# Kernel optimization log

Measured on AMD Instinct MI355X. Metric: run time of the kernel, lower is better.

## Reference

```python
import jax, jax.numpy as jnp
import numpy as np
from jax import lax

N_CLS = 3
ALPHA = 2
NMS = True


def _make_level(key, B, A, D, H, W, P, counts):
    k1, k2, k3, k4, k5 = jax.random.split(key, 5)
    C = N_CLS * A
    logit = jax.random.normal(k1, (B, C, D, H, W), dtype=jnp.float32)
    # valid positive coords use d,h,w >= 1 so padded writes to (0,0,0,0) never collide
    a = jax.random.randint(k2, (B, P), 0, A)
    d = jax.random.randint(k3, (B, P), 1, D)
    h = jax.random.randint(k4, (B, P), 1, H)
    w = jax.random.randint(k5, (B, P), 1, W)
    labels = jax.random.randint(jax.random.fold_in(key, 7), (B, P), 0, N_CLS)
    valid = jnp.arange(P)[None, :] < jnp.asarray(counts)[:, None]  # [B,P]
    coord = jnp.stack([a, d, h, w], axis=-1)
    coord = jnp.where(valid[..., None], coord, -1).astype(jnp.int32)
    # ground-truth prob map: -1 = negative, class id (float) at positive voxels
    prob_gt = -jnp.ones((B, A, D, H, W), dtype=jnp.float32)
    cs = jnp.where(valid[..., None], coord, 0)
    b_idx = jnp.arange(B)[:, None]
    vals = jnp.where(valid, labels.astype(jnp.float32), -1.0)
    prob_gt = prob_gt.at[b_idx, cs[..., 0], cs[..., 1], cs[..., 2], cs[..., 3]].set(vals)
    return logit, prob_gt, coord


def setup_inputs() -> dict:
    key = jax.random.key(0)
    kA, kB = jax.random.split(key)
    logit0, prob_gt0, coord0 = _make_level(kA, 4, 3, 64, 64, 64, 128, [128, 64, 32, 0])
    logit1, prob_gt1, coord1 = _make_level(kB, 4, 3, 32, 32, 32, 128, [64, 16, 8, 128])
    weight_cls = jnp.array([1.0, 1.5, 2.0], dtype=jnp.float32)
    return {
        "logit0": logit0, "logit1": logit1,
        "prob_gt0": prob_gt0, "prob_gt1": prob_gt1,
        "coord0": coord0, "coord1": coord1,
        "weight_cls": weight_cls,
    }


def _level_loss(logit, prob_gt, coord_gt, weight_cls):
    B, C, D, H, W = logit.shape
    A = C // N_CLS
    logit = logit.reshape(B, N_CLS, A, D, H, W)
    logp = jax.nn.log_softmax(logit, axis=1)
    nll = -logp                      # [B,N_cls,A,D,H,W]
    prob = jnp.exp(logp)
    nll_neg = nll[:, 0]              # [B,A,D,H,W]
    prob_neg = prob[:, 0]
    negmask = (prob_gt == -1).astype(logit.dtype)
    if NMS:
        mp = lax.reduce_window(nll_neg, -jnp.inf, lax.max,
                               (1, 1, 3, 3, 3), (1, 1, 1, 1, 1),
                               [(0, 0), (0, 0), (1, 1), (1, 1), (1, 1)])
        negmask = negmask * lax.stop_gradient((mp == nll_neg).astype(logit.dtype))
    w_neg = (1.0 - lax.stop_gradient(prob_neg)) ** ALPHA * negmask
    loss_neg = jnp.sum(nll_neg * w_neg)
    count_neg = jnp.sum(w_neg)
    # positives: ragged coord gather, masked instead of per-sample python loop
    valid = coord_gt[:, :, 0] > -1                       # [B,P]
    c = jnp.where(valid[..., None], coord_gt, 0)         # safe coords
    a, d, h, w = c[..., 0], c[..., 1], c[..., 2], c[..., 3]
    b_idx = jnp.arange(B)[:, None]
    cls = prob_gt[b_idx, a, d, h, w].astype(jnp.int32)   # class id at positives
    cls = jnp.where(valid, cls, 0)
    p_t = prob[b_idx, cls, a, d, h, w]
    nll_t = nll[b_idx, cls, a, d, h, w]
    w_pos = ((1.0 - lax.stop_gradient(p_t)) ** ALPHA
             * weight_cls[cls] * valid.astype(logit.dtype))
    loss_pos = jnp.sum(nll_t * w_pos)
    count_pos = jnp.sum(w_pos)
    return loss_pos, loss_neg, count_pos, count_neg


def reference(logit0, logit1, prob_gt0, prob_gt1, coord0, coord1, weight_cls):
    lp0, ln0, cp0, cn0 = _level_loss(logit0, prob_gt0, coord0, weight_cls)
    lp1, ln1, cp1, cn1 = _level_loss(logit1, prob_gt1, coord1, weight_cls)
    return jnp.stack([lp0 + lp1, ln0 + ln1, cp0 + cp1, cn0 + cn1])
```

## Files before the change

### kernel.cpp

```cpp
#include <hip/hip_runtime.h>
#include <math.h>

#define NEG_INF (-INFINITY)

__device__ __forceinline__ float nll3(float l0, float l1, float l2) {
    float m = fmaxf(l0, fmaxf(l1, l2));
    float e0 = __expf(l0 - m);
    float e1 = __expf(l1 - m);
    float e2 = __expf(l2 - m);
    return __logf(e0 + e1 + e2) - (l0 - m);
}

template<int W, int NR, int TD, int D, int H>
__device__ void neg_strip_p2(int uid, int lane,
                             const float* __restrict__ logit,
                             const float* __restrict__ pg,
                             float2* __restrict__ slot) {
    constexpr int LR = W / 4;
    constexpr int NI = NR + 2;
    constexpr int HG = H / NR;
    constexpr int DT = D / TD;
    const int q = lane % LR;
    const int g = lane / LR;

    int t = uid;
    const int hg = t % HG; t /= HG;
    const int dt = t % DT; t /= DT;
    const int ba = t;
    const int a = ba % 3, b = ba / 3;
    const int h0 = hg * NR, d0 = dt * TD;
    const int HW = H * W;

    const long S = (long)D * HW;
    const float* lb  = logit + ((long)b * 9 + a) * S;
    const long  cs   = 3 * S;
    const float* pgb = pg + (long)ba * S;

    const int jrow = h0 - 1 + g;
    const bool hv = (jrow >= 0) && (jrow < H) && (g < NI);
    const int hcl = min(max(jrow, 0), H - 1);
    const int rowoff = hcl * W + 4 * q;
    const int prowoff = (h0 + min(g, NR - 1)) * W + 4 * q;

    float4 A0, A1, A2, B0, B1, B2, C0, C1, C2;
    float4 GA, GB, GC;
    bool vA, vB, vC;

    {
        const float* p = lb + (long)max(d0 - 1, 0) * HW + rowoff;
        A0 = *(const float4*)p;
        A1 = *(const float4*)(p + cs);
        A2 = *(const float4*)(p + 2 * cs);
        vA = (d0 - 1 >= 0);
        const float* p2 = lb + (long)d0 * HW + rowoff;
        B0 = *(const float4*)p2;
        B1 = *(const float4*)(p2 + cs);
        B2 = *(const float4*)(p2 + 2 * cs);
        vB = true;
        GA = make_float4(0.f, 0.f, 0.f, 0.f);
        GB = make_float4(0.f, 0.f, 0.f, 0.f);
    }

    float vm0[4], vm1[4], cc1[4];
#pragma unroll
    for (int i = 0; i < 4; ++i) { vm0[i] = NEG_INF; vm1[i] = NEG_INF; cc1[i] = 0.f; }

    float loss = 0.f, cnt = 0.f;

#pragma unroll
    for (int s = 0; s <= TD + 1; ++s) {
        if (s <= TD - 1) {
            const int pd = d0 + 1 + s;
            const float* p = lb + (long)min(pd, D - 1) * HW + rowoff;
            C0 = *(const float4*)p;
            C1 = *(const float4*)(p + cs);
            C2 = *(const float4*)(p + 2 * cs);
            vC = (pd < D);
            GC = *(const float4*)(pgb + (long)(d0 + s) * HW + prowoff);
        } else {
            vC = false;
            C0 = C1 = C2 = make_float4(0.f, 0.f, 0.f, 0.f);
            GC = make_float4(0.f, 0.f, 0.f, 0.f);
        }

        float nvv[4];
        {
            const bool vv = vA && hv;
            nvv[0] = vv ? nll3(A0.x, A1.x, A2.x) : NEG_INF;
            nvv[1] = vv ? nll3(A0.y, A1.y, A2.y) : NEG_INF;
            nvv[2] = vv ? nll3(A0.z, A1.z, A2.z) : NEG_INF;
            nvv[3] = vv ? nll3(A0.w, A1.w, A2.w) : NEG_INF;
        }

        float le = __shfl(nvv[3], lane - 1);
        float re = __shfl(nvv[0], lane + 1);
        le = (q == 0)      ? NEG_INF : le;
        re = (q == LR - 1) ? NEG_INF : re;
        float rm[4];
        rm[0] = fmaxf(le,     fmaxf(nvv[0], nvv[1]));
        rm[1] = fmaxf(nvv[0], fmaxf(nvv[1], nvv[2]));
        rm[2] = fmaxf(nvv[1], fmaxf(nvv[2], nvv[3]));
        rm[3] = fmaxf(nvv[2], fmaxf(nvv[3], re));

        float rmA[4], rmB[4], ctr[4];
#pragma unroll
        for (int i = 0; i < 4; ++i) {
            rmA[i] = __shfl(rm[i],  lane + LR);
            rmB[i] = __shfl(rm[i],  lane + 2 * LR);
            ctr[i] = __shfl(nvv[i], lane + LR);
        }

        const float pgv[4] = {GA.x, GA.y, GA.z, GA.w};
#pragma unroll
        for (int i = 0; i < 4; ++i) {
            float hw2 = fmaxf(rm[i], fmaxf(rmA[i], rmB[i]));
            if (s >= 2 && g < NR && pgv[i] == -1.0f) {
                float mp = fmaxf(vm0[i], fmaxf(vm1[i], hw2));
                if (mp == cc1[i]) {
                    float pn = __expf(-cc1[i]);
                    float wn = (1.f - pn) * (1.f - pn);
                    loss += cc1[i] * wn;
                    cnt  += wn;
                }
            }
            vm0[i] = vm1[i]; vm1[i] = hw2; cc1[i] = ctr[i];
        }

        GA = GB; GB = GC;
        A0 = B0; A1 = B1; A2 = B2; vA = vB;
        B0 = C0; B1 = C1; B2 = C2; vB = vC;
    }

#pragma unroll
    for (int off = 32; off > 0; off >>= 1) {
        loss += __shfl_down(loss, off);
        cnt  += __shfl_down(cnt, off);
    }
    if (lane == 0) slot[uid] = make_float2(loss, cnt);
}

__device__ void pos_wave8(int sub, int lane,
                          const float* __restrict__ logit,
                          const float* __restrict__ prob_gt,
                          const int* __restrict__ coord,
                          const float* __restrict__ wcls,
                          float2* __restrict__ slot,
                          int D, int H, int W) {
    const int A = 3, P = 128;
    const long S = (long)D * H * W;
    const int i = sub * 64 + lane;
    const int b = i / P;
    const int* c = coord + (long)i * 4;
    const int a = c[0];
    float loss = 0.f, cnt = 0.f;
    if (a > -1) {
        const int d = c[1], h = c[2], w = c[3];
        const long s = ((long)d * H + h) * W + w;
        const int cls = (int)prob_gt[((long)b * A + a) * S + s];
        const float* lp = logit + ((long)b * 3 * A + a) * S + s;
        float l0 = lp[0];
        float l1 = lp[(long)A * S];
        float l2 = lp[2L * A * S];
        float m = fmaxf(l0, fmaxf(l1, l2));
        float e0 = __expf(l0 - m);
        float e1 = __expf(l1 - m);
        float e2 = __expf(l2 - m);
        float lsum = __logf(e0 + e1 + e2);
        float lc = (cls == 0) ? l0 : ((cls == 1) ? l1 : l2);
        float lpc = (lc - m) - lsum;
        float pt = __expf(lpc);
        float wp = (1.f - pt) * (1.f - pt) * wcls[cls];
        loss = (-lpc) * wp;
        cnt = wp;
    }
#pragma unroll
    for (int off = 32; off > 0; off >>= 1) {
        loss += __shfl_down(loss, off);
        cnt  += __shfl_down(cnt, off);
    }
    if (lane == 0) *slot = make_float2(loss, cnt);
}

#define NW0 3072
#define NW1 384
#define NWP 16
#define NUNEG (NW0 + NW1)
#define TOTAL_WAVES (NW0 + NW1 + NWP)

__global__ __launch_bounds__(256)
void mega_kernel(const float* __restrict__ logit0,
                 const float* __restrict__ logit1,
                 const float* __restrict__ pg0,
                 const float* __restrict__ pg1,
                 const int* __restrict__ coord0,
                 const int* __restrict__ coord1,
                 const float* __restrict__ wcls,
                 float2* __restrict__ ws) {
    const int gw = blockIdx.x * 4 + (threadIdx.x >> 6);
    const int lane = threadIdx.x & 63;
    float2* wsneg = ws;
    float2* wspos = ws + NUNEG;
    if (gw < NW0) {
        neg_strip_p2<64, 2, 8, 64, 64>(gw, lane, logit0, pg0, wsneg);
    } else if (gw < NW0 + NW1) {
        neg_strip_p2<32, 4, 8, 32, 32>(gw - NW0, lane, logit1, pg1, wsneg + NW0);
    } else if (gw < NW0 + NW1 + 8) {
        const int sub = gw - NW0 - NW1;
        pos_wave8(sub, lane, logit0, pg0, coord0, wcls, wspos + sub, 64, 64, 64);
    } else {
        const int sub = gw - NW0 - NW1 - 8;
        pos_wave8(sub, lane, logit1, pg1, coord1, wcls, wspos + 8 + sub, 32, 32, 32);
    }
}

__global__ __launch_bounds__(1024)
void final_reduce(const float2* __restrict__ ws, float* __restrict__ out) {
    const float2* wsneg = ws;
    const float2* wspos = ws + NUNEG;
    float ln = 0.f, cn = 0.f, lp = 0.f, cp = 0.f;
    for (int i = threadIdx.x; i < NUNEG; i += 1024) {
        float2 v = wsneg[i]; ln += v.x; cn += v.y;
    }
    if (threadIdx.x < NWP) {
        float2 v = wspos[threadIdx.x]; lp = v.x; cp = v.y;
    }
#pragma unroll
    for (int off = 32; off > 0; off >>= 1) {
        ln += __shfl_down(ln, off); cn += __shfl_down(cn, off);
        lp += __shfl_down(lp, off); cp += __shfl_down(cp, off);
    }
    __shared__ float s[16][4];
    const int wv = threadIdx.x >> 6;
    if ((threadIdx.x & 63) == 0) {
        s[wv][0] = ln; s[wv][1] = cn; s[wv][2] = lp; s[wv][3] = cp;
    }
    __syncthreads();
    if (threadIdx.x == 0) {
        float a = 0.f, b = 0.f, c = 0.f, d = 0.f;
#pragma unroll
        for (int i = 0; i < 16; ++i) {
            a += s[i][0]; b += s[i][1]; c += s[i][2]; d += s[i][3];
        }
        out[0] = c;
        out[1] = a;
        out[2] = d;
        out[3] = b;
    }
}

extern "C" void kernel_launch(void* const* d_in, const int* in_sizes, int n_in,
                              void* d_out, int out_size, void* d_ws, size_t ws_size,
                              hipStream_t stream) {
    const float* logit0   = (const float*)d_in[0];
    const float* logit1   = (const float*)d_in[1];
    const float* prob_gt0 = (const float*)d_in[2];
    const float* prob_gt1 = (const float*)d_in[3];
    const int*   coord0   = (const int*)d_in[4];
    const int*   coord1   = (const int*)d_in[5];
    const float* wcls     = (const float*)d_in[6];
    float* out = (float*)d_out;
    float2* ws = (float2*)d_ws;

    mega_kernel<<<TOTAL_WAVES / 4, 256, 0, stream>>>(
        logit0, logit1, prob_gt0, prob_gt1, coord0, coord1, wcls, ws);
    final_reduce<<<1, 1024, 0, stream>>>(ws, out);
}
```

Measured before the change: 106.0 us.

## Split NLL computation into a separate pass before NMS strip kernel

After: 108.8 us. +2.6%, slower.

```diff
diff --git a/kernel.cpp b/kernel.cpp
--- a/kernel.cpp
+++ b/kernel.cpp
@@ -11,11 +11,56 @@
     return __logf(e0 + e1 + e2) - (l0 - m);
 }
 
+#define S0 262144
+#define S1 32768
+#define N0 (12 * S0)
+#define N1 (12 * S1)
+#define N0_4 (N0 / 4)
+#define N1_4 (N1 / 4)
+#define P1_BLOCKS ((N0_4 + N1_4) / 256)
+
+__global__ __launch_bounds__(256)
+void nll_pass(const float* __restrict__ logit0,
+              const float* __restrict__ logit1,
+              float* __restrict__ nllws) {
+    const int idx = blockIdx.x * 256 + threadIdx.x;
+    if (idx < N0_4) {
+        const int per = S0 / 4;
+        const int ba = idx / per, r4 = idx % per;
+        const int a = ba % 3, b = ba / 3;
+        const float* p = logit0 + ((long)b * 9 + a) * S0 + (long)r4 * 4;
+        float4 l0 = *(const float4*)p;
+        float4 l1 = *(const float4*)(p + (long)3 * S0);
+        float4 l2 = *(const float4*)(p + (long)6 * S0);
+        float4 o;
+        o.x = nll3(l0.x, l1.x, l2.x);
+        o.y = nll3(l0.y, l1.y, l2.y);
+        o.z = nll3(l0.z, l1.z, l2.z);
+        o.w = nll3(l0.w, l1.w, l2.w);
+        *(float4*)(nllws + (long)ba * S0 + (long)r4 * 4) = o;
+    } else {
+        const int j = idx - N0_4;
+        const int per = S1 / 4;
+        const int ba = j / per, r4 = j % per;
+        const int a = ba % 3, b = ba / 3;
+        const float* p = logit1 + ((long)b * 9 + a) * S1 + (long)r4 * 4;
+        float4 l0 = *(const float4*)p;
+        float4 l1 = *(const float4*)(p + (long)3 * S1);
+        float4 l2 = *(const float4*)(p + (long)6 * S1);
+        float4 o;
+        o.x = nll3(l0.x, l1.x, l2.x);
+        o.y = nll3(l0.y, l1.y, l2.y);
+        o.z = nll3(l0.z, l1.z, l2.z);
+        o.w = nll3(l0.w, l1.w, l2.w);
+        *(float4*)(nllws + N0 + (long)ba * S1 + (long)r4 * 4) = o;
+    }
+}
+
 template<int W, int NR, int TD, int D, int H>
-__device__ void neg_strip_p2(int uid, int lane,
-                             const float* __restrict__ logit,
-                             const float* __restrict__ pg,
-                             float2* __restrict__ slot) {
+__device__ void nms_strip(int uid, int lane,
+                          const float* __restrict__ nlvl,
+                          const float* __restrict__ pg,
+                          float2* __restrict__ slot) {
     constexpr int LR = W / 4;
     constexpr int NI = NR + 2;
     constexpr int HG = H / NR;
@@ -27,13 +72,10 @@
     const int hg = t % HG; t /= HG;
     const int dt = t % DT; t /= DT;
     const int ba = t;
-    const int a = ba % 3, b = ba / 3;
     const int h0 = hg * NR, d0 = dt * TD;
     const int HW = H * W;
-
     const long S = (long)D * HW;
-    const float* lb  = logit + ((long)b * 9 + a) * S;
-    const long  cs   = 3 * S;
+    const float* nb  = nlvl + (long)ba * S;
     const float* pgb = pg + (long)ba * S;
 
     const int jrow = h0 - 1 + g;
@@ -42,24 +84,13 @@
     const int rowoff = hcl * W + 4 * q;
     const int prowoff = (h0 + min(g, NR - 1)) * W + 4 * q;
 
-    float4 A0, A1, A2, B0, B1, B2, C0, C1, C2;
-    float4 GA, GB, GC;
-    bool vA, vB, vC;
-
-    {
-        const float* p = lb + (long)max(d0 - 1, 0) * HW + rowoff;
-        A0 = *(const float4*)p;
-        A1 = *(const float4*)(p + cs);
-        A2 = *(const float4*)(p + 2 * cs);
-        vA = (d0 - 1 >= 0);
-        const float* p2 = lb + (long)d0 * HW + rowoff;
-        B0 = *(const float4*)p2;
-        B1 = *(const float4*)(p2 + cs);
-        B2 = *(const float4*)(p2 + 2 * cs);
-        vB = true;
-        GA = make_float4(0.f, 0.f, 0.f, 0.f);
-        GB = make_float4(0.f, 0.f, 0.f, 0.f);
-    }
+    float4 nl[3]; bool vd[3]; float4 pq[3];
+    nl[0] = *(const float4*)(nb + (long)max(d0 - 1, 0) * HW + rowoff);
+    vd[0] = (d0 - 1 >= 0);
+    nl[1] = *(const float4*)(nb + (long)d0 * HW + rowoff);
+    vd[1] = true;
+    nl[2] = make_float4(0.f, 0.f, 0.f, 0.f); vd[2] = false;
+    pq[0] = pq[1] = pq[2] = make_float4(0.f, 0.f, 0.f, 0.f);
 
     float vm0[4], vm1[4], cc1[4];
 #pragma unroll
@@ -71,26 +102,18 @@
     for (int s = 0; s <= TD + 1; ++s) {
         if (s <= TD - 1) {
             const int pd = d0 + 1 + s;
-            const float* p = lb + (long)min(pd, D - 1) * HW + rowoff;
-            C0 = *(const float4*)p;
-            C1 = *(const float4*)(p + cs);
-            C2 = *(const float4*)(p + 2 * cs);
-            vC = (pd < D);
-            GC = *(const float4*)(pgb + (long)(d0 + s) * HW + prowoff);
-        } else {
-            vC = false;
-            C0 = C1 = C2 = make_float4(0.f, 0.f, 0.f, 0.f);
-            GC = make_float4(0.f, 0.f, 0.f, 0.f);
-        }
-
+            nl[(s + 2) % 3] = *(const float4*)(nb + (long)min(pd, D - 1) * HW + rowoff);
+            vd[(s + 2) % 3] = (pd < D);
+            pq[s % 3] = *(const float4*)(pgb + (long)(d0 + s) * HW + prowoff);
+        }
+
+        const float4 cv = nl[s % 3];
+        const bool vv = vd[s % 3] && hv;
         float nvv[4];
-        {
-            const bool vv = vA && hv;
-            nvv[0] = vv ? nll3(A0.x, A1.x, A2.x) : NEG_INF;
-            nvv[1] = vv ? nll3(A0.y, A1.y, A2.y) : NEG_INF;
-            nvv[2] = vv ? nll3(A0.z, A1.z, A2.z) : NEG_INF;
-            nvv[3] = vv ? nll3(A0.w, A1.w, A2.w) : NEG_INF;
-        }
+        nvv[0] = vv ? cv.x : NEG_INF;
+        nvv[1] = vv ? cv.y : NEG_INF;
+        nvv[2] = vv ? cv.z : NEG_INF;
+        nvv[3] = vv ? cv.w : NEG_INF;
 
         float le = __shfl(nvv[3], lane - 1);
         float re = __shfl(nvv[0], lane + 1);
@@ -110,7 +133,8 @@
             ctr[i] = __shfl(nvv[i], lane + LR);
         }
 
-        const float pgv[4] = {GA.x, GA.y, GA.z, GA.w};
+        const float4 gp = pq[(s + 1) % 3];
+        const float pgv[4] = {gp.x, gp.y, gp.z, gp.w};
 #pragma unroll
         for (int i = 0; i < 4; ++i) {
             float hw2 = fmaxf(rm[i], fmaxf(rmA[i], rmB[i]));
@@ -125,10 +149,6 @@
             }
             vm0[i] = vm1[i]; vm1[i] = hw2; cc1[i] = ctr[i];
         }
-
-        GA = GB; GB = GC;
-        A0 = B0; A1 = B1; A2 = B2; vA = vB;
-        B0 = C0; B1 = C1; B2 = C2; vB = vC;
     }
 
 #pragma unroll
@@ -184,45 +204,44 @@
 #define NW0 3072
 #define NW1 384
 #define NWP 16
-#define NUNEG (NW0 + NW1)
+#define NSLOT_NEG (NW0 + NW1)
 #define TOTAL_WAVES (NW0 + NW1 + NWP)
 
 __global__ __launch_bounds__(256)
-void mega_kernel(const float* __restrict__ logit0,
-                 const float* __restrict__ logit1,
-                 const float* __restrict__ pg0,
-                 const float* __restrict__ pg1,
-                 const int* __restrict__ coord0,
-                 const int* __restrict__ coord1,
-                 const float* __restrict__ wcls,
-                 float2* __restrict__ ws) {
+void nms_pass(const float* __restrict__ nllws,
+              const float* __restrict__ logit0,
+              const float* __restrict__ logit1,
+              const float* __restrict__ pg0,
+              const float* __restrict__ pg1,
+              const int* __restrict__ coord0,
+              const int* __restrict__ coord1,
+              const float* __restrict__ wcls,
+              float2* __restrict__ slots) {
     const int gw = blockIdx.x * 4 + (threadIdx.x >> 6);
     const int lane = threadIdx.x & 63;
-    float2* wsneg = ws;
-    float2* wspos = ws + NUNEG;
     if (gw < NW0) {
-        neg_strip_p2<64, 2, 8, 64, 64>(gw, lane, logit0, pg0, wsneg);
+        nms_strip<64, 2, 8, 64, 64>(gw, lane, nllws, pg0, slots);
     } else if (gw < NW0 + NW1) {
-        neg_strip_p2<32, 4, 8, 32, 32>(gw - NW0, lane, logit1, pg1, wsneg + NW0);
+        nms_strip<32, 4, 8, 32, 32>(gw - NW0, lane, nllws + N0, pg1, slots + NW0);
     } else if (gw < NW0 + NW1 + 8) {
         const int sub = gw - NW0 - NW1;
-        pos_wave8(sub, lane, logit0, pg0, coord0, wcls, wspos + sub, 64, 64, 64);
+        pos_wave8(sub, lane, logit0, pg0, coord0, wcls,
+                  slots + NSLOT_NEG + sub, 64, 64, 64);
     } else {
         const int sub = gw - NW0 - NW1 - 8;
-        pos_wave8(sub, lane, logit1, pg1, coord1, wcls, wspos + 8 + sub, 32, 32, 32);
+        pos_wave8(sub, lane, logit1, pg1, coord1, wcls,
+                  slots + NSLOT_NEG + 8 + sub, 32, 32, 32);
     }
 }
 
 __global__ __launch_bounds__(1024)
-void final_reduce(const float2* __restrict__ ws, float* __restrict__ out) {
-    const float2* wsneg = ws;
-    const float2* wspos = ws + NUNEG;
+void final_reduce(const float2* __restrict__ slots, float* __restrict__ out) {
     float ln = 0.f, cn = 0.f, lp = 0.f, cp = 0.f;
-    for (int i = threadIdx.x; i < NUNEG; i += 1024) {
-        float2 v = wsneg[i]; ln += v.x; cn += v.y;
+    for (int i = threadIdx.x; i < NSLOT_NEG; i += 1024) {
+        float2 v = slots[i]; ln += v.x; cn += v.y;
     }
     if (threadIdx.x < NWP) {
-        float2 v = wspos[threadIdx.x]; lp = v.x; cp = v.y;
+        float2 v = slots[NSLOT_NEG + threadIdx.x]; lp = v.x; cp = v.y;
     }
 #pragma unroll
     for (int off = 32; off > 0; off >>= 1) {
@@ -259,9 +278,12 @@
     const int*   coord1   = (const int*)d_in[5];
     const float* wcls     = (const float*)d_in[6];
     float* out = (float*)d_out;
-    float2* ws = (float2*)d_ws;
-
-    mega_kernel<<<TOTAL_WAVES / 4, 256, 0, stream>>>(
-        logit0, logit1, prob_gt0, prob_gt1, coord0, coord1, wcls, ws);
-    final_reduce<<<1, 1024, 0, stream>>>(ws, out);
-}
+
+    float*  nllws = (float*)d_ws;
+    float2* slots = (float2*)(nllws + N0 + N1);
+
+    nll_pass<<<P1_BLOCKS, 256, 0, stream>>>(logit0, logit1, nllws);
+    nms_pass<<<TOTAL_WAVES / 4, 256, 0, stream>>>(
+        nllws, logit0, logit1, prob_gt0, prob_gt1, coord0, coord1, wcls, slots);
+    final_reduce<<<1, 1024, 0, stream>>>(slots, out);
+}
```
